# Performance work log

Hardware: AMD Instinct MI355X
Metric: run time of the kernel (lower is better)

The kernel has to match this reference:

```python
import jax, jax.numpy as jnp
import numpy as np

L, E, H, V = 12, 1024, 4096, 50277
LN_EPS = 9.999999747378752e-06  # tf float32 1e-5


def _layernorm(x, w, b):
    m = jnp.mean(x)
    xc = x - m
    return xc / jnp.sqrt(jnp.mean(xc * xc) + LN_EPS) * w + b


def setup_inputs() -> dict:
    key = jax.random.key(0)
    ks = jax.random.split(key, 32)
    f32 = jnp.float32

    def n(i, shape, s=0.02):
        return (jax.random.normal(ks[i], shape, f32) * s).astype(f32)

    inp = {
        "statea": n(0, (L, E), 0.3),
        "stateb": jax.random.uniform(ks[1], (L, E), f32),
        "statec": jax.random.uniform(ks[2], (L, E), f32),
        "stated": n(3, (L, E), 0.3),
        "preprocess": n(4, (V, E), 0.5),
        "ln1w": 1.0 + n(5, (L, E), 0.05),
        "ln1b": n(6, (L, E), 0.05),
        "ln2w": 1.0 + n(7, (L, E), 0.05),
        "ln2b": n(8, (L, E), 0.05),
        "att_key": n(9, (L, E, E)),
        "att_receptance": n(10, (L, E, E)),
        "att_value": n(11, (L, E, E)),
        "kktk": jax.random.uniform(ks[12], (L, E), f32),
        "vvtv": jax.random.uniform(ks[13], (L, E), f32),
        "rrtr": jax.random.uniform(ks[14], (L, E), f32),
        "time_first": n(15, (L, E), 0.2),
        "time_decay": n(16, (L, E), 0.2) - 1.0,
        "outputvv": n(17, (L, E, E)),
        "time_mix_k_ffn": jax.random.uniform(ks[18], (L, E), f32),
        "time_mix_r_ffn": jax.random.uniform(ks[19], (L, E), f32),
        "key_ffn": n(20, (L, H, E)),
        "receptance_ffn": n(21, (L, E, E)),
        "value_ffn": n(22, (L, E, H)),
        "post0": 1.0 + n(23, (E,), 0.05),
        "post1": n(24, (E,), 0.05),
        "post2": n(25, (V, E)),
        "token": 123,
    }
    return inp


def _forward(statea, stateb, statec, stated, preprocess, ln1w, ln1b, ln2w, ln2b,
             att_key, att_receptance, att_value, kktk, vvtv, rrtr, time_first,
             time_decay, outputvv, time_mix_k_ffn, time_mix_r_ffn, key_ffn,
             receptance_ffn, value_ffn, post0, post1, post2, token):
    x0 = preprocess[token]  # [E]

    def step(x, p):
        (sa, sb, sc, sd, l1w, l1b, l2w, l2b, ak, ar, av, kk, vv, rr,
         tfirst, tdecay, ovv, tmk_m, tmr_m, kf, rf, vf) = p
        xy = _layernorm(x, l1w, l1b)
        # WKV time-mixing (single step): mat-vecs + exp-decay state recursion
        k = jnp.exp(ak @ (xy + kk * sa))        # [E]
        v = av @ (xy + vv * sa)                 # [E]
        r = jnp.exp(ar @ (xy + rr * sa)) + 1.0  # [E]
        etf = jnp.exp(tfirst)
        w = sb + etf * k * v
        d = sc * r + etf * k * r
        mvv = ovv @ (w / (d + 0.001))           # [E]
        sxx = x + mvv
        aaa = xy
        etd = jnp.exp(tdecay)
        bbb = sb * etd + k * v
        ccc = sc * etd + k
        # channel-mixing FFN
        xx = _layernorm(sxx, l2w, l2b)
        kma = kf @ (xx + tmk_m * sd)            # [H]
        km = jnp.square(jnp.maximum(kma, 0.0))
        rt = jnp.exp(rf @ (xx + tmr_m * sd)) + 1.0  # [E]
        x_new = sxx + (vf @ km) / rt
        ddd = xx
        return x_new, (aaa, bbb, ccc, ddd)

    xs = (statea, stateb, statec, stated, ln1w, ln1b, ln2w, ln2b, att_key,
          att_receptance, att_value, kktk, vvtv, rrtr, time_first, time_decay,
          outputvv, time_mix_k_ffn, time_mix_r_ffn, key_ffn, receptance_ffn,
          value_ffn)
    xL, (aaa, bbb, ccc, ddd) = jax.lax.scan(step, x0, xs)
    logits = post2 @ _layernorm(xL, post0, post1)  # [V]
    return logits, aaa, bbb, ccc, ddd


def reference(statea, stateb, statec, stated, preprocess, ln1w, ln1b, ln2w, ln2b,
              att_key, att_receptance, att_value, kktk, vvtv, rrtr, time_first,
              time_decay, outputvv, time_mix_k_ffn, time_mix_r_ffn, key_ffn,
              receptance_ffn, value_ffn, post0, post1, post2, token):
    return _forward(statea, stateb, statec, stated, preprocess, ln1w, ln1b,
                    ln2w, ln2b, att_key, att_receptance, att_value, kktk, vvtv,
                    rrtr, time_first, time_decay, outputvv, time_mix_k_ffn,
                    time_mix_r_ffn, key_ffn, receptance_ffn, value_ffn, post0,
                    post1, post2, token)
```

## Files before the change

### kernel.cpp

```cpp
#include <hip/hip_runtime.h>
#include <math.h>


constexpr int E = 1024;
constexpr int H = 4096;
constexpr int V = 50277;
constexpr int L = 12;
constexpr int NBLK = 256;
constexpr int NTHR = 512;
constexpr float LN_EPS = 9.999999747378752e-06f;

#define SCOPE_AGENT __HIP_MEMORY_SCOPE_AGENT

__device__ __forceinline__ void cstoref(float *p, float v) {
  __hip_atomic_store(p, v, __ATOMIC_RELAXED, SCOPE_AGENT);
}
__device__ __forceinline__ float cloadf(const float *p) {
  return __hip_atomic_load(p, __ATOMIC_RELAXED, SCOPE_AGENT);
}
__device__ __forceinline__ void cstoreu(unsigned *p, unsigned v) {
  __hip_atomic_store(p, v, __ATOMIC_RELAXED, SCOPE_AGENT);
}
__device__ __forceinline__ unsigned cloadu(const unsigned *p) {
  return __hip_atomic_load(p, __ATOMIC_RELAXED, SCOPE_AGENT);
}

struct Args {
  const float *statea, *stateb, *statec, *stated, *pre;
  const float *ln1w, *ln1b, *ln2w, *ln2b;
  const float *ak, *ar, *av, *kk, *vv, *rr, *tf, *td, *ovv;
  const float *tmk, *tmr, *kf, *rf, *vf;
  const float *post0, *post1, *post2;
  const int *token;
  float *out;
  float *ws;
  unsigned *gen;
  unsigned *flags;
};

__device__ __forceinline__ void bar_arrive(const Args &a, unsigned ep, int blk) {
  __syncthreads();
  if (blk != 0 && threadIdx.x == 0) cstoreu(&a.flags[blk * 32], ep);
}

__device__ __forceinline__ void bar_wait(const Args &a, unsigned ep, int blk) {
  if (blk == 0) {
    int t = threadIdx.x;
    if (t > 0 && t < NBLK) {
      while (cloadu(&a.flags[t * 32]) < ep) {}
    }
    __syncthreads();
    if (t == 0) cstoreu(a.gen, ep);
  } else {
    if (threadIdx.x == 0) {
      while (cloadu(a.gen) < ep) __builtin_amdgcn_s_sleep(1);
    }
    __syncthreads();
  }
}

__device__ __forceinline__ float wred(float v) {
#pragma unroll
  for (int off = 32; off; off >>= 1) v += __shfl_down(v, off, 64);
  return v;
}

__device__ __forceinline__ float dot4(float4 w, float4 x) {
  return w.x * x.x + w.y * x.y + w.z * x.z + w.w * x.w;
}

__device__ __forceinline__ float2 block_stats_v(float2 v, float *s_x, float *s_red,
                                                int tid, int lane, int wid) {
  reinterpret_cast<float2 *>(s_x)[tid] = v;
  float s = v.x + v.y, s2 = v.x * v.x + v.y * v.y;
#pragma unroll
  for (int off = 32; off; off >>= 1) {
    s += __shfl_down(s, off, 64);
    s2 += __shfl_down(s2, off, 64);
  }
  if (lane == 0) { s_red[wid] = s; s_red[8 + wid] = s2; }
  __syncthreads();
  float ts = 0.f, ts2 = 0.f;
#pragma unroll
  for (int i = 0; i < 8; ++i) { ts += s_red[i]; ts2 += s_red[8 + i]; }
  float m = ts * (1.0f / E);
  float var = ts2 * (1.0f / E) - m * m;
  return make_float2(m, rsqrtf(var + LN_EPS));
}

__global__ __launch_bounds__(NTHR) void rwkv_fused(Args a) {
  __shared__ __align__(16) float s_a[4096];
  __shared__ __align__(16) float s_x[1024];
  __shared__ __align__(16) float s_y[1024];
  __shared__ float s_pp[24];
  __shared__ float s_red[16];
  __shared__ float s_rt[4];

  const int tid = threadIdx.x;
  const int lane = tid & 63;
  const int wid = tid >> 6;
  const int blk = blockIdx.x;
  const int rloc = wid >> 1;
  const int h = wid & 1;
  const int grow = blk * 4 + rloc;

  float *ws_u = a.ws, *ws_sxx = a.ws + 1024, *ws_x = a.ws + 2048, *ws_km = a.ws + 3072;
  float *out_logits = a.out;
  float *out_aaa = a.out + V;
  float *out_bbb = out_aaa + L * E;
  float *out_ccc = out_bbb + L * E;
  float *out_ddd = out_ccc + L * E;

  const int tok = a.token[0];
  const float *pre_row = a.pre + (size_t)tok * E;
  const float4 *s4a = reinterpret_cast<const float4 *>(s_a);

  float4 pw[10];
  unsigned ep = 1;

  {
    const float4 *kr = reinterpret_cast<const float4 *>(a.ak + (size_t)grow * E);
    const float4 *vr = reinterpret_cast<const float4 *>(a.av + (size_t)grow * E);
    const float4 *rr = reinterpret_cast<const float4 *>(a.ar + (size_t)grow * E);
    int b0 = h * 128 + lane;
    pw[0] = kr[b0]; pw[1] = kr[b0 + 64];
    pw[2] = vr[b0]; pw[3] = vr[b0 + 64];
    pw[4] = rr[b0]; pw[5] = rr[b0 + 64];
    asm volatile("" ::: "memory");
  }

  for (int l = 0; l < L; ++l) {
    const size_t lE = (size_t)l * E;

    {
      float2 v;
      if (l == 0) {
        v = reinterpret_cast<const float2 *>(pre_row)[tid];
      } else {
        v.x = cloadf(ws_x + 2 * tid);
        v.y = cloadf(ws_x + 2 * tid + 1);
      }
      float2 st = block_stats_v(v, s_x, s_red, tid, lane, wid);
#pragma unroll
      for (int j = 0; j < 2; ++j) {
        int e = tid + 512 * j;
        float xy = (s_x[e] - st.x) * st.y * a.ln1w[lE + e] + a.ln1b[lE + e];
        s_y[e] = xy;
        float sa = a.statea[lE + e];
        s_a[e] = xy + a.kk[lE + e] * sa;
        s_a[1024 + e] = xy + a.vv[lE + e] * sa;
        s_a[2048 + e] = xy + a.rr[lE + e] * sa;
      }
      __syncthreads();
      int b0 = h * 128 + lane;
      float accK = dot4(pw[0], s4a[b0]) + dot4(pw[1], s4a[b0 + 64]);
      float accV = dot4(pw[2], s4a[256 + b0]) + dot4(pw[3], s4a[256 + b0 + 64]);
      float accR = dot4(pw[4], s4a[512 + b0]) + dot4(pw[5], s4a[512 + b0 + 64]);
      accK = wred(accK); accV = wred(accV); accR = wred(accR);
      if (lane == 0) {
        s_pp[wid * 3 + 0] = accK;
        s_pp[wid * 3 + 1] = accV;
        s_pp[wid * 3 + 2] = accR;
      }
      __syncthreads();
      if (tid < 4) {
        size_t o = lE + blk * 4 + tid;
        float K = s_pp[(2 * tid) * 3] + s_pp[(2 * tid + 1) * 3];
        float Vv = s_pp[(2 * tid) * 3 + 1] + s_pp[(2 * tid + 1) * 3 + 1];
        float R = s_pp[(2 * tid) * 3 + 2] + s_pp[(2 * tid + 1) * 3 + 2];
        float kx = expf(K), rx = expf(R) + 1.0f;
        float etf = expf(a.tf[o]), etd = expf(a.td[o]);
        float sb = a.stateb[o], sc = a.statec[o];
        float w_ = sb + etf * kx * Vv;
        float d_ = sc * rx + etf * kx * rx;
        cstoref(&ws_u[blk * 4 + tid], w_ / (d_ + 0.001f));
        out_bbb[o] = sb * etd + kx * Vv;
        out_ccc[o] = sc * etd + kx;
        out_aaa[o] = s_y[blk * 4 + tid];
      }
    }
    bar_arrive(a, ep, blk);
    {
      const float4 *orow = reinterpret_cast<const float4 *>(a.ovv + (lE + grow) * E);
      int b0 = h * 128 + lane;
      pw[0] = orow[b0]; pw[1] = orow[b0 + 64];
      asm volatile("" ::: "memory");
    }
    bar_wait(a, ep, blk); ++ep;

    {
      s_a[2 * tid] = cloadf(ws_u + 2 * tid);
      s_a[2 * tid + 1] = cloadf(ws_u + 2 * tid + 1);
      __syncthreads();
      int b0 = h * 128 + lane;
      float acc = dot4(pw[0], s4a[b0]) + dot4(pw[1], s4a[b0 + 64]);
      acc = wred(acc);
      if (lane == 0) s_pp[wid] = acc;
      __syncthreads();
      if (tid < 4) {
        float sxx = s_x[blk * 4 + tid] + s_pp[2 * tid] + s_pp[2 * tid + 1];
        cstoref(&ws_sxx[blk * 4 + tid], sxx);
      }
    }
    bar_arrive(a, ep, blk);
    {
      const float *kfb = a.kf + (size_t)l * H * E;
      const float4 *k0 = reinterpret_cast<const float4 *>(kfb + (size_t)(blk * 16 + wid) * E);
      const float4 *k1 = reinterpret_cast<const float4 *>(kfb + (size_t)(blk * 16 + 8 + wid) * E);
      pw[0] = k0[lane];       pw[1] = k0[lane + 64];
      pw[2] = k0[lane + 128]; pw[3] = k0[lane + 192];
      pw[4] = k1[lane];       pw[5] = k1[lane + 64];
      pw[6] = k1[lane + 128]; pw[7] = k1[lane + 192];
      const float4 *rrow = reinterpret_cast<const float4 *>(a.rf + (lE + grow) * E);
      int b0 = h * 128 + lane;
      pw[8] = rrow[b0]; pw[9] = rrow[b0 + 64];
      asm volatile("" ::: "memory");
    }
    bar_wait(a, ep, blk); ++ep;

    {
      float2 v;
      v.x = cloadf(ws_sxx + 2 * tid);
      v.y = cloadf(ws_sxx + 2 * tid + 1);
      float2 st = block_stats_v(v, s_x, s_red, tid, lane, wid);
#pragma unroll
      for (int j = 0; j < 2; ++j) {
        int e = tid + 512 * j;
        float xx = (s_x[e] - st.x) * st.y * a.ln2w[lE + e] + a.ln2b[lE + e];
        s_y[e] = xx;
        float sd = a.stated[lE + e];
        s_a[e] = xx + a.tmk[lE + e] * sd;
        s_a[1024 + e] = xx + a.tmr[lE + e] * sd;
      }
      __syncthreads();
      float k0 = dot4(pw[0], s4a[lane]) + dot4(pw[1], s4a[lane + 64]) +
                 dot4(pw[2], s4a[lane + 128]) + dot4(pw[3], s4a[lane + 192]);
      float k1 = dot4(pw[4], s4a[lane]) + dot4(pw[5], s4a[lane + 64]) +
                 dot4(pw[6], s4a[lane + 128]) + dot4(pw[7], s4a[lane + 192]);
      int b0 = h * 128 + lane;
      float ar_ = dot4(pw[8], s4a[256 + b0]) + dot4(pw[9], s4a[256 + b0 + 64]);
      k0 = wred(k0); k1 = wred(k1); ar_ = wred(ar_);
      if (lane == 0) {
        float t0 = fmaxf(k0, 0.f), t1 = fmaxf(k1, 0.f);
        cstoref(&ws_km[blk * 16 + wid], t0 * t0);
        cstoref(&ws_km[blk * 16 + 8 + wid], t1 * t1);
        s_pp[wid] = ar_;
      }
      __syncthreads();
      if (tid < 4) {
        s_rt[tid] = expf(s_pp[2 * tid] + s_pp[2 * tid + 1]) + 1.0f;
        out_ddd[lE + blk * 4 + tid] = s_y[blk * 4 + tid];
      }
    }
    bar_arrive(a, ep, blk);
    {
      const float4 *vrow = reinterpret_cast<const float4 *>(a.vf + (lE + grow) * H);
      int b0 = h * 512 + lane;
      pw[0] = vrow[b0];       pw[1] = vrow[b0 + 64];
      pw[2] = vrow[b0 + 128]; pw[3] = vrow[b0 + 192];
      pw[4] = vrow[b0 + 256]; pw[5] = vrow[b0 + 320];
      pw[6] = vrow[b0 + 384]; pw[7] = vrow[b0 + 448];
      asm volatile("" ::: "memory");
    }
    bar_wait(a, ep, blk); ++ep;

    {
#pragma unroll
      for (int j = 0; j < 8; ++j)
        s_a[tid + 512 * j] = cloadf(ws_km + tid + 512 * j);
      __syncthreads();
      int b0 = h * 512 + lane;
      float acc = dot4(pw[0], s4a[b0]) + dot4(pw[1], s4a[b0 + 64]) +
                  dot4(pw[2], s4a[b0 + 128]) + dot4(pw[3], s4a[b0 + 192]) +
                  dot4(pw[4], s4a[b0 + 256]) + dot4(pw[5], s4a[b0 + 320]) +
                  dot4(pw[6], s4a[b0 + 384]) + dot4(pw[7], s4a[b0 + 448]);
      acc = wred(acc);
      if (lane == 0) s_pp[wid] = acc;
      __syncthreads();
      if (tid < 4) {
        float xn = s_x[blk * 4 + tid] + (s_pp[2 * tid] + s_pp[2 * tid + 1]) / s_rt[tid];
        cstoref(&ws_x[blk * 4 + tid], xn);
      }
    }
    bar_arrive(a, ep, blk);
    if (l < L - 1) {
      const size_t lE2 = (size_t)(l + 1) * E;
      const float4 *kr = reinterpret_cast<const float4 *>(a.ak + (lE2 + grow) * E);
      const float4 *vr = reinterpret_cast<const float4 *>(a.av + (lE2 + grow) * E);
      const float4 *rr = reinterpret_cast<const float4 *>(a.ar + (lE2 + grow) * E);
      int b0 = h * 128 + lane;
      pw[0] = kr[b0]; pw[1] = kr[b0 + 64];
      pw[2] = vr[b0]; pw[3] = vr[b0 + 64];
      pw[4] = rr[b0]; pw[5] = rr[b0 + 64];
      asm volatile("" ::: "memory");
    }
    bar_wait(a, ep, blk); ++ep;
  }

  {
    float2 v;
    v.x = cloadf(ws_x + 2 * tid);
    v.y = cloadf(ws_x + 2 * tid + 1);
    float2 st = block_stats_v(v, s_x, s_red, tid, lane, wid);
#pragma unroll
    for (int j = 0; j < 2; ++j) {
      int e = tid + 512 * j;
      s_a[e] = (s_x[e] - st.x) * st.y * a.post0[e] + a.post1[e];
    }
    __syncthreads();

    int gw = blk * 8 + wid;
    for (int r0 = gw; r0 < V; r0 += 4096) {
      int r1 = r0 + 2048;
      bool hasB = r1 < V;
      const float4 *p0 = reinterpret_cast<const float4 *>(a.post2 + (size_t)r0 * E);
      const float4 *p1 = reinterpret_cast<const float4 *>(a.post2 + (size_t)(hasB ? r1 : r0) * E);
      float a0 = dot4(p0[lane], s4a[lane]) + dot4(p0[lane + 64], s4a[lane + 64]) +
                 dot4(p0[lane + 128], s4a[lane + 128]) + dot4(p0[lane + 192], s4a[lane + 192]);
      float a1 = dot4(p1[lane], s4a[lane]) + dot4(p1[lane + 64], s4a[lane + 64]) +
                 dot4(p1[lane + 128], s4a[lane + 128]) + dot4(p1[lane + 192], s4a[lane + 192]);
      a0 = wred(a0); a1 = wred(a1);
      if (lane == 0) {
        out_logits[r0] = a0;
        if (hasB) out_logits[r1] = a1;
      }
    }
  }
}

extern "C" void kernel_launch(void *const *d_in, const int *in_sizes, int n_in,
                              void *d_out, int out_size, void *d_ws, size_t ws_size,
                              hipStream_t stream) {
  (void)in_sizes; (void)n_in; (void)out_size; (void)ws_size;
  Args a;
  a.statea = (const float *)d_in[0];
  a.stateb = (const float *)d_in[1];
  a.statec = (const float *)d_in[2];
  a.stated = (const float *)d_in[3];
  a.pre    = (const float *)d_in[4];
  a.ln1w   = (const float *)d_in[5];
  a.ln1b   = (const float *)d_in[6];
  a.ln2w   = (const float *)d_in[7];
  a.ln2b   = (const float *)d_in[8];
  a.ak     = (const float *)d_in[9];
  a.ar     = (const float *)d_in[10];
  a.av     = (const float *)d_in[11];
  a.kk     = (const float *)d_in[12];
  a.vv     = (const float *)d_in[13];
  a.rr     = (const float *)d_in[14];
  a.tf     = (const float *)d_in[15];
  a.td     = (const float *)d_in[16];
  a.ovv    = (const float *)d_in[17];
  a.tmk    = (const float *)d_in[18];
  a.tmr    = (const float *)d_in[19];
  a.kf     = (const float *)d_in[20];
  a.rf     = (const float *)d_in[21];
  a.vf     = (const float *)d_in[22];
  a.post0  = (const float *)d_in[23];
  a.post1  = (const float *)d_in[24];
  a.post2  = (const float *)d_in[25];
  a.token  = (const int *)d_in[26];
  a.out    = (float *)d_out;

  a.gen    = (unsigned *)d_ws;
  a.flags  = (unsigned *)((char *)d_ws + 128);
  a.ws     = (float *)((char *)d_ws + 36864);

  hipMemsetAsync(d_ws, 0, 36864, stream);
  rwkv_fused<<<NBLK, NTHR, 0, stream>>>(a);
}
```

Baseline: 275.1 us.

## Decentralize grid barrier, vectorize coherent loads, prefetch logits rows

Replaces the master-block grid barrier with an all-to-all flag barrier: every block publishes its epoch flag and polls all 256 flags directly, which removes one hop through a generation counter. Cross-block workspace reads now use vectorized inline-asm loads with sc0 sc1 cache bypass instead of scalar atomic loads. The final logits mat-vec loop is software-pipelined so the next rows of post2 are loaded while the current ones are reduced. Polling all 256 flags from every block adds memory traffic, and the inline asm carries its own waitcnt handling.

```diff
diff --git a/kernel.cpp b/kernel.cpp
--- a/kernel.cpp
+++ b/kernel.cpp
@@ -15,14 +15,26 @@
 __device__ __forceinline__ void cstoref(float *p, float v) {
   __hip_atomic_store(p, v, __ATOMIC_RELAXED, SCOPE_AGENT);
 }
-__device__ __forceinline__ float cloadf(const float *p) {
-  return __hip_atomic_load(p, __ATOMIC_RELAXED, SCOPE_AGENT);
-}
 __device__ __forceinline__ void cstoreu(unsigned *p, unsigned v) {
   __hip_atomic_store(p, v, __ATOMIC_RELAXED, SCOPE_AGENT);
 }
 __device__ __forceinline__ unsigned cloadu(const unsigned *p) {
   return __hip_atomic_load(p, __ATOMIC_RELAXED, SCOPE_AGENT);
+}
+
+__device__ __forceinline__ float2 cload2(const void *p) {
+  float2 r;
+  asm volatile("global_load_dwordx2 %0, %1, off sc0 sc1\n\t"
+               "s_waitcnt vmcnt(0)"
+               : "=&v"(r) : "v"(p) : "memory");
+  return r;
+}
+__device__ __forceinline__ void cload4x2(float4 &r0, float4 &r1,
+                                         const void *p0, const void *p1) {
+  asm volatile("global_load_dwordx4 %0, %2, off sc0 sc1\n\t"
+               "global_load_dwordx4 %1, %3, off sc0 sc1\n\t"
+               "s_waitcnt vmcnt(0)"
+               : "=&v"(r0), "=&v"(r1) : "v"(p0), "v"(p1) : "memory");
 }
 
 struct Args {
@@ -34,29 +46,20 @@
   const int *token;
   float *out;
   float *ws;
-  unsigned *gen;
   unsigned *flags;
 };
 
 __device__ __forceinline__ void bar_arrive(const Args &a, unsigned ep, int blk) {
   __syncthreads();
-  if (blk != 0 && threadIdx.x == 0) cstoreu(&a.flags[blk * 32], ep);
-}
-
-__device__ __forceinline__ void bar_wait(const Args &a, unsigned ep, int blk) {
-  if (blk == 0) {
-    int t = threadIdx.x;
-    if (t > 0 && t < NBLK) {
-      while (cloadu(&a.flags[t * 32]) < ep) {}
-    }
-    __syncthreads();
-    if (t == 0) cstoreu(a.gen, ep);
-  } else {
-    if (threadIdx.x == 0) {
-      while (cloadu(a.gen) < ep) __builtin_amdgcn_s_sleep(1);
-    }
-    __syncthreads();
-  }
+  if (threadIdx.x == 0) cstoreu(&a.flags[blk * 32], ep);
+}
+
+__device__ __forceinline__ void bar_wait(const Args &a, unsigned ep) {
+  if (threadIdx.x < NBLK) {
+    while (cloadu(&a.flags[threadIdx.x * 32]) < ep)
+      __builtin_amdgcn_s_sleep(2);
+  }
+  __syncthreads();
 }
 
 __device__ __forceinline__ float wred(float v) {
@@ -86,6 +89,11 @@
   float m = ts * (1.0f / E);
   float var = ts2 * (1.0f / E) - m * m;
   return make_float2(m, rsqrtf(var + LN_EPS));
+}
+
+__device__ __forceinline__ void loadrow(float4 *d, const float4 *P, int r, int lane) {
+  const float4 *p = P + (size_t)r * 256;
+  d[0] = p[lane]; d[1] = p[lane + 64]; d[2] = p[lane + 128]; d[3] = p[lane + 192];
 }
 
 __global__ __launch_bounds__(NTHR) void rwkv_fused(Args a) {
@@ -137,8 +145,7 @@
       if (l == 0) {
         v = reinterpret_cast<const float2 *>(pre_row)[tid];
       } else {
-        v.x = cloadf(ws_x + 2 * tid);
-        v.y = cloadf(ws_x + 2 * tid + 1);
+        v = cload2(reinterpret_cast<const float2 *>(ws_x) + tid);
       }
       float2 st = block_stats_v(v, s_x, s_red, tid, lane, wid);
 #pragma unroll
@@ -186,11 +193,11 @@
       pw[0] = orow[b0]; pw[1] = orow[b0 + 64];
       asm volatile("" ::: "memory");
     }
-    bar_wait(a, ep, blk); ++ep;
-
-    {
-      s_a[2 * tid] = cloadf(ws_u + 2 * tid);
-      s_a[2 * tid + 1] = cloadf(ws_u + 2 * tid + 1);
+    bar_wait(a, ep); ++ep;
+
+    {
+      reinterpret_cast<float2 *>(s_a)[tid] =
+          cload2(reinterpret_cast<const float2 *>(ws_u) + tid);
       __syncthreads();
       int b0 = h * 128 + lane;
       float acc = dot4(pw[0], s4a[b0]) + dot4(pw[1], s4a[b0 + 64]);
@@ -216,12 +223,10 @@
       pw[8] = rrow[b0]; pw[9] = rrow[b0 + 64];
       asm volatile("" ::: "memory");
     }
-    bar_wait(a, ep, blk); ++ep;
-
-    {
-      float2 v;
-      v.x = cloadf(ws_sxx + 2 * tid);
-      v.y = cloadf(ws_sxx + 2 * tid + 1);
+    bar_wait(a, ep); ++ep;
+
+    {
+      float2 v = cload2(reinterpret_cast<const float2 *>(ws_sxx) + tid);
       float2 st = block_stats_v(v, s_x, s_red, tid, lane, wid);
 #pragma unroll
       for (int j = 0; j < 2; ++j) {
@@ -262,12 +267,15 @@
       pw[6] = vrow[b0 + 384]; pw[7] = vrow[b0 + 448];
       asm volatile("" ::: "memory");
     }
-    bar_wait(a, ep, blk); ++ep;
-
-    {
-#pragma unroll
-      for (int j = 0; j < 8; ++j)
-        s_a[tid + 512 * j] = cloadf(ws_km + tid + 512 * j);
+    bar_wait(a, ep); ++ep;
+
+    {
+      float4 km0, km1;
+      cload4x2(km0, km1,
+               reinterpret_cast<const float4 *>(ws_km) + tid,
+               reinterpret_cast<const float4 *>(ws_km) + tid + 512);
+      reinterpret_cast<float4 *>(s_a)[tid] = km0;
+      reinterpret_cast<float4 *>(s_a)[tid + 512] = km1;
       __syncthreads();
       int b0 = h * 512 + lane;
       float acc = dot4(pw[0], s4a[b0]) + dot4(pw[1], s4a[b0 + 64]) +
@@ -294,13 +302,11 @@
       pw[4] = rr[b0]; pw[5] = rr[b0 + 64];
       asm volatile("" ::: "memory");
     }
-    bar_wait(a, ep, blk); ++ep;
+    bar_wait(a, ep); ++ep;
   }
 
   {
-    float2 v;
-    v.x = cloadf(ws_x + 2 * tid);
-    v.y = cloadf(ws_x + 2 * tid + 1);
+    float2 v = cload2(reinterpret_cast<const float2 *>(ws_x) + tid);
     float2 st = block_stats_v(v, s_x, s_red, tid, lane, wid);
 #pragma unroll
     for (int j = 0; j < 2; ++j) {
@@ -309,21 +315,33 @@
     }
     __syncthreads();
 
-    int gw = blk * 8 + wid;
-    for (int r0 = gw; r0 < V; r0 += 4096) {
-      int r1 = r0 + 2048;
-      bool hasB = r1 < V;
-      const float4 *p0 = reinterpret_cast<const float4 *>(a.post2 + (size_t)r0 * E);
-      const float4 *p1 = reinterpret_cast<const float4 *>(a.post2 + (size_t)(hasB ? r1 : r0) * E);
-      float a0 = dot4(p0[lane], s4a[lane]) + dot4(p0[lane + 64], s4a[lane + 64]) +
-                 dot4(p0[lane + 128], s4a[lane + 128]) + dot4(p0[lane + 192], s4a[lane + 192]);
-      float a1 = dot4(p1[lane], s4a[lane]) + dot4(p1[lane + 64], s4a[lane + 64]) +
-                 dot4(p1[lane + 128], s4a[lane + 128]) + dot4(p1[lane + 192], s4a[lane + 192]);
+    const float4 *P2 = reinterpret_cast<const float4 *>(a.post2);
+    const int gw = blk * 8 + wid;
+    int r0 = gw, r1 = gw + 2048;
+    float4 A0[4], A1[4];
+    loadrow(A0, P2, r0, lane);
+    loadrow(A1, P2, r1 < V ? r1 : r0, lane);
+    while (true) {
+      int n0 = r0 + 4096, n1 = n0 + 2048;
+      bool more = n0 < V;
+      float4 B0[4], B1[4];
+      if (more) {
+        loadrow(B0, P2, n0, lane);
+        loadrow(B1, P2, n1 < V ? n1 : n0, lane);
+      }
+      float a0 = dot4(A0[0], s4a[lane]) + dot4(A0[1], s4a[lane + 64]) +
+                 dot4(A0[2], s4a[lane + 128]) + dot4(A0[3], s4a[lane + 192]);
+      float a1 = dot4(A1[0], s4a[lane]) + dot4(A1[1], s4a[lane + 64]) +
+                 dot4(A1[2], s4a[lane + 128]) + dot4(A1[3], s4a[lane + 192]);
       a0 = wred(a0); a1 = wred(a1);
       if (lane == 0) {
         out_logits[r0] = a0;
-        if (hasB) out_logits[r1] = a1;
-      }
+        if (r1 < V) out_logits[r1] = a1;
+      }
+      if (!more) break;
+#pragma unroll
+      for (int q = 0; q < 4; ++q) { A0[q] = B0[q]; A1[q] = B1[q]; }
+      r0 = n0; r1 = n1;
     }
   }
 }
@@ -362,10 +380,9 @@
   a.token  = (const int *)d_in[26];
   a.out    = (float *)d_out;
 
-  a.gen    = (unsigned *)d_ws;
-  a.flags  = (unsigned *)((char *)d_ws + 128);
-  a.ws     = (float *)((char *)d_ws + 36864);
-
-  hipMemsetAsync(d_ws, 0, 36864, stream);
+  a.flags  = (unsigned *)d_ws;
+  a.ws     = (float *)((char *)d_ws + 32768);
+
+  hipMemsetAsync(d_ws, 0, 32768, stream);
   rwkv_fused<<<NBLK, NTHR, 0, stream>>>(a);
 }
```

Result: faster. 242.4 us (-11.9%).
